# Kernel tuning notes

Measured on AMD Instinct MI355X. Metric: run time of the kernel, lower is better.

The kernel has to match this reference:

```python
import jax, jax.numpy as jnp
import numpy as np

_EPSILON = 1e-06

def _sparsemax(z):
    # sparsemax along last axis (Martins & Astudillo 2016, sort-based projection)
    m = z.shape[-1]
    z_sorted = jnp.flip(jnp.sort(z, axis=-1), axis=-1)          # descending
    z_cum = jnp.cumsum(z_sorted, axis=-1)
    r = jnp.arange(1, m + 1, dtype=z.dtype)
    support = (1.0 + r * z_sorted) > z_cum                       # [b, m]
    k = jnp.sum(support, axis=-1, keepdims=True)                 # support size, int
    tau = (jnp.take_along_axis(z_cum, k - 1, axis=-1) - 1.0) / k.astype(z.dtype)
    return jnp.maximum(z - tau, 0.0)

def setup_inputs() -> dict:
    key = jax.random.key(0)
    ks = jax.random.split(key, 4)
    b, m, d, out = 2048, 8192, 1024, 1000
    encoder_output = jax.random.normal(ks[0], (b, d), dtype=jnp.float32)
    memory_set = jax.random.normal(ks[1], (m, d), dtype=jnp.float32)
    W1 = jax.random.normal(ks[2], (d, 2 * d), dtype=jnp.float32) * (1.0 / np.sqrt(d))
    b1 = jnp.zeros((2 * d,), dtype=jnp.float32)
    W2 = jax.random.normal(ks[3], (2 * d, out), dtype=jnp.float32) * (1.0 / np.sqrt(2 * d))
    b2 = jnp.zeros((out,), dtype=jnp.float32)
    return {"encoder_output": encoder_output, "memory_set": memory_set,
            "W1": W1, "b1": b1, "W2": W2, "b2": b2}

def reference(encoder_output, memory_set, W1, b1, W2, b2):
    # cosine distance: 1 - x_hat @ y_hat^T  (with eps inside the sqrt, as in torch code)
    x_norm = encoder_output / jnp.sqrt(jnp.sum(encoder_output * encoder_output, axis=1, keepdims=True) + _EPSILON)
    y_norm = memory_set / jnp.sqrt(jnp.sum(memory_set * memory_set, axis=1, keepdims=True) + _EPSILON)
    dist = 1.0 - jnp.matmul(x_norm, y_norm.T)                    # [b, m]
    content_weights = _sparsemax(-dist)                          # [b, m]
    memory_vector = jnp.matmul(content_weights, memory_set)      # [b, d]
    h = jax.nn.relu(jnp.matmul(memory_vector, W1) + b1)          # [b, 2d]
    output = jnp.matmul(h, W2) + b2                              # [b, out]
    return output
```

## Files before the change

### kernel.cpp

```cpp
#include <hip/hip_runtime.h>
#include <hip/hip_bf16.h>


#define TPB 256
#define CAP 1024

typedef __bf16 bf16x8 __attribute__((ext_vector_type(8)));
typedef float  f32x4  __attribute__((ext_vector_type(4)));

typedef const __attribute__((address_space(1))) void* gas_ptr;
typedef __attribute__((address_space(3))) void*       las_ptr;

__device__ __forceinline__ unsigned short f2bf(float f) {
    __hip_bfloat16 h = __float2bfloat16(f);
    union { __hip_bfloat16 h; unsigned short s; } u; u.h = h; return u.s;
}

__device__ __forceinline__ float bf2f(unsigned short s) {
    union { unsigned int b; float f; } u; u.b = (unsigned int)s << 16; return u.f;
}

__device__ __forceinline__ float block_reduce_sum(float v, float* sred) {
    #pragma unroll
    for (int off = 32; off > 0; off >>= 1) v += __shfl_down(v, off, 64);
    int lane = threadIdx.x & 63;
    int wid  = threadIdx.x >> 6;
    if (lane == 0) sred[wid] = v;
    __syncthreads();
    if (threadIdx.x == 0) {
        float s = 0.f;
        for (int i = 0; i < 4; ++i) s += sred[i];
        sred[0] = s;
    }
    __syncthreads();
    float r = sred[0];
    __syncthreads();
    return r;
}

__device__ __forceinline__ void block_reduce_sum2(float& a, float& b, float* sred) {
    #pragma unroll
    for (int off = 32; off > 0; off >>= 1) {
        a += __shfl_down(a, off, 64);
        b += __shfl_down(b, off, 64);
    }
    int lane = threadIdx.x & 63, wid = threadIdx.x >> 6;
    if (lane == 0) { sred[wid] = a; sred[4 + wid] = b; }
    __syncthreads();
    if (threadIdx.x == 0) {
        sred[0] = sred[0] + sred[1] + sred[2] + sred[3];
        sred[4] = sred[4] + sred[5] + sred[6] + sred[7];
    }
    __syncthreads();
    a = sred[0]; b = sred[4];
    __syncthreads();
}

__global__ __launch_bounds__(TPB) void normalize_rows_bf16(const float* __restrict__ X,
                                                           unsigned short* __restrict__ Y,
                                                           float* __restrict__ norms,
                                                           int cols) {
    __shared__ float sred[4];
    int row = blockIdx.x, tid = threadIdx.x;
    const float4* x4 = (const float4*)(X + (size_t)row * cols);
    ushort4* y4 = (ushort4*)(Y + (size_t)row * cols);
    int n4 = cols >> 2;
    float ss = 0.f;
    for (int i = tid; i < n4; i += TPB) {
        float4 v = x4[i];
        ss += v.x * v.x + v.y * v.y + v.z * v.z + v.w * v.w;
    }
    float tot = block_reduce_sum(ss, sred);
    float nrm = sqrtf(tot + 1e-6f);
    float inv = 1.0f / nrm;
    if (norms && tid == 0) norms[row] = nrm;
    for (int i = tid; i < n4; i += TPB) {
        float4 v = x4[i];
        ushort4 o;
        o.x = f2bf(v.x * inv); o.y = f2bf(v.y * inv);
        o.z = f2bf(v.z * inv); o.w = f2bf(v.w * inv);
        y4[i] = o;
    }
}

__global__ __launch_bounds__(TPB) void transpose_cast(const float* __restrict__ in,
                                                      unsigned short* __restrict__ out,
                                                      int R, int C, int Cpad) {
    __shared__ float t[32][33];
    int x = threadIdx.x & 31, y = threadIdx.x >> 5;
    int r0 = blockIdx.y * 32, c0 = blockIdx.x * 32;
    #pragma unroll
    for (int yy = y; yy < 32; yy += 8) {
        int c = c0 + x;
        t[yy][x] = (c < C) ? in[(size_t)(r0 + yy) * C + c] : 0.f;
    }
    __syncthreads();
    #pragma unroll
    for (int yy = y; yy < 32; yy += 8) {
        int c = c0 + yy;
        if (c < Cpad)
            out[(size_t)c * R + r0 + x] = f2bf(t[x][yy]);
    }
}

__global__ __launch_bounds__(TPB) void sparsemax_compact(float* __restrict__ Z,
                                                         const float* __restrict__ ynorm,
                                                         int* __restrict__ cnt, int m) {
    __shared__ float sz[8192];
    __shared__ float sred[8];
    __shared__ unsigned short cidx[CAP];
    __shared__ float cval[CAP];
    __shared__ unsigned int lcnt, ocnt;
    int row = blockIdx.x, tid = threadIdx.x;
    float* zrow = Z + (size_t)row * m;
    unsigned int* prow = (unsigned int*)zrow;
    int n4 = m >> 2;
    float4* sz4 = (float4*)sz;
    const float4* zr4 = (const float4*)zrow;

    float s = 0.f, q = 0.f;
    for (int i = tid; i < n4; i += TPB) {
        float4 v = zr4[i];
        sz4[i] = v;
        s += v.x + v.y + v.z + v.w;
        q += v.x * v.x + v.y * v.y + v.z * v.z + v.w * v.w;
    }
    if (tid == 0) { lcnt = 0; ocnt = 0; }
    block_reduce_sum2(s, q, sred);
    float fm   = (float)m;
    float mean = s / fm;
    float sig  = sqrtf(fmaxf(q / fm - mean * mean, 0.f));
    float tau_s = (s - 1.f) / fm;
    float tau_g = mean + 2.f * sig;

    float Sg = 0.f, cg = 0.f, Ss = 0.f, cs = 0.f;
    for (int i = tid; i < m; i += TPB) {
        float z = sz[i];
        if (z > tau_g) { Sg += z - tau_g; cg += 1.f; }
        if (z > tau_s) { Ss += z - tau_s; cs += 1.f; }
    }
    block_reduce_sum2(Sg, cg, sred);
    block_reduce_sum2(Ss, cs, sred);

    float tau_lb, S_act, c_act;
    if (Sg >= 1.f) { tau_lb = tau_g; S_act = Sg + cg * tau_g; c_act = cg; }
    else           { tau_lb = tau_s; S_act = Ss + cs * tau_s; c_act = cs; }
    float tau1 = (S_act - 1.f) / c_act;
    if (tau1 < tau_lb) tau1 = tau_lb;

    for (int i = tid; i < m; i += TPB) {
        float z = sz[i];
        if (z > tau1) {
            unsigned int slot = atomicAdd(&lcnt, 1u);
            if (slot < CAP) { cidx[slot] = (unsigned short)i; cval[slot] = z; }
        }
    }
    __syncthreads();

    if (lcnt <= CAP && lcnt > 0) {
        int n = (int)lcnt;
        float tau = tau1, prev = -1.f;
        for (int it = 0; it < 64; ++it) {
            float S = 0.f, c = 0.f;
            for (int j = tid; j < n; j += TPB) {
                float z = cval[j];
                if (z > tau) { S += z; c += 1.f; }
            }
            block_reduce_sum2(S, c, sred);
            if (c < 0.5f || c == prev) break;
            tau = (S - 1.f) / c; prev = c;
        }
        for (int j = tid; j < n; j += TPB) {
            float w = cval[j] - tau;
            if (w > 0.f) {
                int idx = (int)cidx[j];
                unsigned int slot = atomicAdd(&ocnt, 1u);
                prow[slot] = ((unsigned int)idx << 16) | (unsigned int)f2bf(w * ynorm[idx]);
            }
        }
        __syncthreads();
        if (tid == 0) cnt[row] = (int)ocnt;
    } else {
        float tau = tau1, prev = -1.f;
        for (int it = 0; it < 64; ++it) {
            float S = 0.f, c = 0.f;
            for (int i = tid; i < m; i += TPB) {
                float z = sz[i];
                if (z > tau) { S += z; c += 1.f; }
            }
            block_reduce_sum2(S, c, sred);
            if (c < 0.5f || c == prev) break;
            tau = (S - 1.f) / c; prev = c;
        }
        for (int i = tid; i < m; i += TPB) {
            float w = sz[i] - tau;
            if (w > 0.f) {
                unsigned int slot = atomicAdd(&ocnt, 1u);
                prow[slot] = ((unsigned int)i << 16) | (unsigned int)f2bf(w * ynorm[i]);
            }
        }
        __syncthreads();
        if (tid == 0) cnt[row] = (int)ocnt;
    }
}

__global__ __launch_bounds__(TPB) void sparse_mv(const unsigned int* __restrict__ packed,
                                                 const int* __restrict__ cnt,
                                                 const unsigned short* __restrict__ yn,
                                                 unsigned short* __restrict__ mv,
                                                 int m, int d) {
    __shared__ unsigned int sl[TPB];
    int row = blockIdx.x, tid = threadIdx.x;
    const unsigned int* prow = packed + (size_t)row * m;
    int n = cnt[row];
    int c0 = tid * 4;
    float acc0 = 0.f, acc1 = 0.f, acc2 = 0.f, acc3 = 0.f;
    for (int j0 = 0; j0 < n; j0 += TPB) {
        int chunk = min(TPB, n - j0);
        __syncthreads();
        if (tid < chunk) sl[tid] = prow[j0 + tid];
        __syncthreads();
        #pragma unroll 4
        for (int jj = 0; jj < chunk; ++jj) {
            unsigned int u = sl[jj];
            int idx = (int)(u >> 16);
            float w = bf2f((unsigned short)(u & 0xffffu));
            ushort4 v = *(const ushort4*)&yn[(size_t)idx * d + c0];
            acc0 += w * bf2f(v.x);
            acc1 += w * bf2f(v.y);
            acc2 += w * bf2f(v.z);
            acc3 += w * bf2f(v.w);
        }
    }
    ushort4 o;
    o.x = f2bf(acc0); o.y = f2bf(acc1); o.z = f2bf(acc2); o.w = f2bf(acc3);
    *(ushort4*)&mv[(size_t)row * d + c0] = o;
}

template <int BN, int STORE_BF16, int RELU, int HASBIAS>
__global__ __launch_bounds__(TPB) void gemm_bt(const unsigned short* __restrict__ A,
                                               const unsigned short* __restrict__ B,
                                               const float* __restrict__ bias,
                                               void* __restrict__ C,
                                               int M, int K, int lda, int NOUT, int ldc) {
    constexpr int IT = (BN == 128) ? 4 : 2;
    __shared__ unsigned short lA[128 * 32];
    __shared__ unsigned short lB[BN * 32];
    int tid = threadIdx.x;
    int lane = tid & 63, wv = tid >> 6;
    int wm = (BN == 128) ? (wv & 1) * 64 : wv * 32;
    int wn = (BN == 128) ? (wv >> 1) * 64 : 0;
    int lr = lane & 15, kq = lane >> 4;

    int rowBase = blockIdx.y * 128;
    int colBase = blockIdx.x * BN;

    f32x4 acc[IT][4] = {};

    for (int k0 = 0; k0 < K; k0 += 32) {
        #pragma unroll
        for (int l = 0; l < 2; ++l) {
            int li = l * 256 + tid;
            int r = li >> 2, seg = li & 3;
            const char* g = (const char*)(A + (size_t)(rowBase + r) * lda + k0) + seg * 16;
            __builtin_amdgcn_global_load_lds((gas_ptr)g, (las_ptr)((char*)lA + li * 16), 16, 0, 0);
        }
        #pragma unroll
        for (int l = 0; l < BN / 64; ++l) {
            int li = l * 256 + tid;
            int r = li >> 2, seg = li & 3;
            const char* g = (const char*)(B + (size_t)(colBase + r) * K + k0) + seg * 16;
            __builtin_amdgcn_global_load_lds((gas_ptr)g, (las_ptr)((char*)lB + li * 16), 16, 0, 0);
        }
        __syncthreads();

        bf16x8 av[IT], bv[4];
        #pragma unroll
        for (int i = 0; i < IT; ++i)
            av[i] = *(const bf16x8*)&lA[(wm + i * 16 + lr) * 32 + kq * 8];
        #pragma unroll
        for (int j = 0; j < 4; ++j)
            bv[j] = *(const bf16x8*)&lB[(wn + j * 16 + lr) * 32 + kq * 8];
        #pragma unroll
        for (int i = 0; i < IT; ++i)
            #pragma unroll
            for (int j = 0; j < 4; ++j)
                acc[i][j] = __builtin_amdgcn_mfma_f32_16x16x32_bf16(av[i], bv[j], acc[i][j], 0, 0, 0);
        __syncthreads();
    }

    float* Cf = (float*)C;
    unsigned short* Cb = (unsigned short*)C;
    #pragma unroll
    for (int j = 0; j < 4; ++j) {
        int col = colBase + wn + j * 16 + lr;
        if (col >= NOUT) continue;
        float bv_ = HASBIAS ? bias[col] : 0.f;
        #pragma unroll
        for (int i = 0; i < IT; ++i) {
            #pragma unroll
            for (int r = 0; r < 4; ++r) {
                int row = rowBase + wm + i * 16 + kq * 4 + r;
                float v = acc[i][j][r] + bv_;
                if (RELU) v = fmaxf(v, 0.f);
                if (STORE_BF16) Cb[(size_t)row * ldc + col] = f2bf(v);
                else            Cf[(size_t)row * ldc + col] = v;
            }
        }
    }
}

extern "C" void kernel_launch(void* const* d_in, const int* in_sizes, int n_in,
                              void* d_out, int out_size, void* d_ws, size_t ws_size,
                              hipStream_t stream) {
    const float* enc = (const float*)d_in[0];
    const float* mem = (const float*)d_in[1];
    const float* W1  = (const float*)d_in[2];
    const float* b1  = (const float*)d_in[3];
    const float* W2  = (const float*)d_in[4];
    const float* b2  = (const float*)d_in[5];

    const int d    = in_sizes[3] / 2;
    const int b    = in_sizes[0] / d;
    const int m    = in_sizes[1] / d;
    const int d2   = in_sizes[3];
    const int outN = in_sizes[5];
    const int outPad = 1024;

    unsigned short* xn    = (unsigned short*)d_ws;
    unsigned short* yn    = xn  + (size_t)b * d;
    float*          ynorm = (float*)(yn + (size_t)m * d);
    unsigned short* W1T   = (unsigned short*)(ynorm + m);
    unsigned short* W2T   = W1T + (size_t)d2 * d;
    float*          Z     = (float*)(W2T + (size_t)outPad * d2);
    int*            cnt   = (int*)(Z + (size_t)b * m);
    unsigned short* mv    = (unsigned short*)(cnt + b);
    unsigned short* h     = mv + (size_t)b * d;

    normalize_rows_bf16<<<b, TPB, 0, stream>>>(enc, xn, nullptr, d);
    normalize_rows_bf16<<<m, TPB, 0, stream>>>(mem, yn, ynorm, d);

    transpose_cast<<<dim3(d2 / 32, d / 32), TPB, 0, stream>>>(W1, W1T, d, d2, d2);
    transpose_cast<<<dim3(outPad / 32, d2 / 32), TPB, 0, stream>>>(W2, W2T, d2, outN, outPad);

    gemm_bt<128, 0, 0, 0><<<dim3(m / 128, b / 128), TPB, 0, stream>>>(xn, yn, nullptr, Z,
                                                                      b, d, d, m, m);
    sparsemax_compact<<<b, TPB, 0, stream>>>(Z, ynorm, cnt, m);

    sparse_mv<<<b, TPB, 0, stream>>>((const unsigned int*)Z, cnt, yn, mv, m, d);

    gemm_bt<64, 1, 1, 1><<<dim3(d2 / 64, b / 128), TPB, 0, stream>>>(mv, W1T, b1, h,
                                                                     b, d, d, d2, d2);
    gemm_bt<64, 0, 0, 1><<<dim3(outPad / 64, b / 128), TPB, 0, stream>>>(h, W2T, b2, d_out,
                                                                         b, d2, d2, outN, outN);
}
```

Baseline: 302.3 us.

## Store similarity matrix in fp16, widen GEMM K-tile with swizzled LDS, merge normalize launches

The similarity GEMM now writes its output as fp16 instead of fp32, halving the write and re-read traffic of the large b×m intermediate. The sparsemax kernel reads it as packed halves, and the sparse-mv pitch is adjusted because the packed index/weight list now lives in the fp16 buffer. The GEMM K-tile grows from 32 to 64, with an XOR swizzle on the LDS layout to avoid bank conflicts, and the two row-normalize launches are merged into one. fp16 rounding of the similarity scores may shift sparsemax support decisions. The packed output rows are also half as long, so a row with a large support could overflow its buffer.

```diff
diff --git a/kernel.cpp b/kernel.cpp
--- a/kernel.cpp
+++ b/kernel.cpp
@@ -4,6 +4,7 @@
 
 #define TPB 256
 #define CAP 1024
+#define BK 64
 
 typedef __bf16 bf16x8 __attribute__((ext_vector_type(8)));
 typedef float  f32x4  __attribute__((ext_vector_type(4)));
@@ -15,23 +16,23 @@
     __hip_bfloat16 h = __float2bfloat16(f);
     union { __hip_bfloat16 h; unsigned short s; } u; u.h = h; return u.s;
 }
-
 __device__ __forceinline__ float bf2f(unsigned short s) {
     union { unsigned int b; float f; } u; u.b = (unsigned int)s << 16; return u.f;
 }
+__device__ __forceinline__ unsigned short f2h(float f) {
+    union { _Float16 h; unsigned short s; } u; u.h = (_Float16)f; return u.s;
+}
+__device__ __forceinline__ float h2f(unsigned short s) {
+    union { unsigned short s; _Float16 h; } u; u.s = s; return (float)u.h;
+}
 
 __device__ __forceinline__ float block_reduce_sum(float v, float* sred) {
     #pragma unroll
     for (int off = 32; off > 0; off >>= 1) v += __shfl_down(v, off, 64);
-    int lane = threadIdx.x & 63;
-    int wid  = threadIdx.x >> 6;
+    int lane = threadIdx.x & 63, wid = threadIdx.x >> 6;
     if (lane == 0) sred[wid] = v;
     __syncthreads();
-    if (threadIdx.x == 0) {
-        float s = 0.f;
-        for (int i = 0; i < 4; ++i) s += sred[i];
-        sred[0] = s;
-    }
+    if (threadIdx.x == 0) sred[0] = sred[0] + sred[1] + sred[2] + sred[3];
     __syncthreads();
     float r = sred[0];
     __syncthreads();
@@ -56,12 +57,17 @@
     __syncthreads();
 }
 
-__global__ __launch_bounds__(TPB) void normalize_rows_bf16(const float* __restrict__ X,
-                                                           unsigned short* __restrict__ Y,
-                                                           float* __restrict__ norms,
-                                                           int cols) {
+__global__ __launch_bounds__(TPB) void normalize_rows_bf16(const float* __restrict__ X0,
+                                                           unsigned short* __restrict__ Y0,
+                                                           const float* __restrict__ X1,
+                                                           unsigned short* __restrict__ Y1,
+                                                           float* __restrict__ norms1,
+                                                           int nrow0, int cols) {
     __shared__ float sred[4];
-    int row = blockIdx.x, tid = threadIdx.x;
+    int r = blockIdx.x, tid = threadIdx.x;
+    const float* X; unsigned short* Y; float* nn; int row;
+    if (r < nrow0) { X = X0; Y = Y0; nn = nullptr; row = r; }
+    else           { X = X1; Y = Y1; nn = norms1; row = r - nrow0; }
     const float4* x4 = (const float4*)(X + (size_t)row * cols);
     ushort4* y4 = (ushort4*)(Y + (size_t)row * cols);
     int n4 = cols >> 2;
@@ -73,7 +79,7 @@
     float tot = block_reduce_sum(ss, sred);
     float nrm = sqrtf(tot + 1e-6f);
     float inv = 1.0f / nrm;
-    if (norms && tid == 0) norms[row] = nrm;
+    if (nn && tid == 0) nn[row] = nrm;
     for (int i = tid; i < n4; i += TPB) {
         float4 v = x4[i];
         ushort4 o;
@@ -103,7 +109,7 @@
     }
 }
 
-__global__ __launch_bounds__(TPB) void sparsemax_compact(float* __restrict__ Z,
+__global__ __launch_bounds__(TPB) void sparsemax_compact(unsigned short* __restrict__ Zh,
                                                          const float* __restrict__ ynorm,
                                                          int* __restrict__ cnt, int m) {
     __shared__ float sz[8192];
@@ -112,18 +118,24 @@
     __shared__ float cval[CAP];
     __shared__ unsigned int lcnt, ocnt;
     int row = blockIdx.x, tid = threadIdx.x;
-    float* zrow = Z + (size_t)row * m;
+    unsigned short* zrow = Zh + (size_t)row * m;
     unsigned int* prow = (unsigned int*)zrow;
-    int n4 = m >> 2;
+    const uint4* zr8 = (const uint4*)zrow;
+    int n8 = m >> 3;
+
+    float s = 0.f, q = 0.f;
     float4* sz4 = (float4*)sz;
-    const float4* zr4 = (const float4*)zrow;
-
-    float s = 0.f, q = 0.f;
-    for (int i = tid; i < n4; i += TPB) {
-        float4 v = zr4[i];
-        sz4[i] = v;
-        s += v.x + v.y + v.z + v.w;
-        q += v.x * v.x + v.y * v.y + v.z * v.z + v.w * v.w;
+    for (int i = tid; i < n8; i += TPB) {
+        uint4 v = zr8[i];
+        float4 a, bq;
+        a.x = h2f((unsigned short)(v.x & 0xffffu)); a.y = h2f((unsigned short)(v.x >> 16));
+        a.z = h2f((unsigned short)(v.y & 0xffffu)); a.w = h2f((unsigned short)(v.y >> 16));
+        bq.x = h2f((unsigned short)(v.z & 0xffffu)); bq.y = h2f((unsigned short)(v.z >> 16));
+        bq.z = h2f((unsigned short)(v.w & 0xffffu)); bq.w = h2f((unsigned short)(v.w >> 16));
+        sz4[2 * i] = a; sz4[2 * i + 1] = bq;
+        s += a.x + a.y + a.z + a.w + bq.x + bq.y + bq.z + bq.w;
+        q += a.x * a.x + a.y * a.y + a.z * a.z + a.w * a.w
+           + bq.x * bq.x + bq.y * bq.y + bq.z * bq.z + bq.w * bq.w;
     }
     if (tid == 0) { lcnt = 0; ocnt = 0; }
     block_reduce_sum2(s, q, sred);
@@ -208,10 +220,10 @@
                                                  const int* __restrict__ cnt,
                                                  const unsigned short* __restrict__ yn,
                                                  unsigned short* __restrict__ mv,
-                                                 int m, int d) {
+                                                 int pitchU, int d) {
     __shared__ unsigned int sl[TPB];
     int row = blockIdx.x, tid = threadIdx.x;
-    const unsigned int* prow = packed + (size_t)row * m;
+    const unsigned int* prow = packed + (size_t)row * pitchU;
     int n = cnt[row];
     int c0 = tid * 4;
     float acc0 = 0.f, acc1 = 0.f, acc2 = 0.f, acc3 = 0.f;
@@ -237,15 +249,15 @@
     *(ushort4*)&mv[(size_t)row * d + c0] = o;
 }
 
-template <int BN, int STORE_BF16, int RELU, int HASBIAS>
+template <int BN, int OUTMODE, int RELU, int HASBIAS>
 __global__ __launch_bounds__(TPB) void gemm_bt(const unsigned short* __restrict__ A,
                                                const unsigned short* __restrict__ B,
                                                const float* __restrict__ bias,
                                                void* __restrict__ C,
                                                int M, int K, int lda, int NOUT, int ldc) {
     constexpr int IT = (BN == 128) ? 4 : 2;
-    __shared__ unsigned short lA[128 * 32];
-    __shared__ unsigned short lB[BN * 32];
+    __shared__ unsigned short lA[128 * BK];
+    __shared__ unsigned short lB[BN * BK];
     int tid = threadIdx.x;
     int lane = tid & 63, wv = tid >> 6;
     int wm = (BN == 128) ? (wv & 1) * 64 : wv * 32;
@@ -257,35 +269,46 @@
 
     f32x4 acc[IT][4] = {};
 
-    for (int k0 = 0; k0 < K; k0 += 32) {
+    for (int k0 = 0; k0 < K; k0 += BK) {
         #pragma unroll
-        for (int l = 0; l < 2; ++l) {
+        for (int l = 0; l < 4; ++l) {
             int li = l * 256 + tid;
-            int r = li >> 2, seg = li & 3;
-            const char* g = (const char*)(A + (size_t)(rowBase + r) * lda + k0) + seg * 16;
+            int row = li >> 3, s0 = li & 7;
+            int seg = s0 ^ (row & 7);
+            const char* g = (const char*)(A + (size_t)(rowBase + row) * lda + k0) + seg * 16;
             __builtin_amdgcn_global_load_lds((gas_ptr)g, (las_ptr)((char*)lA + li * 16), 16, 0, 0);
         }
         #pragma unroll
-        for (int l = 0; l < BN / 64; ++l) {
+        for (int l = 0; l < BN / 32; ++l) {
             int li = l * 256 + tid;
-            int r = li >> 2, seg = li & 3;
-            const char* g = (const char*)(B + (size_t)(colBase + r) * K + k0) + seg * 16;
+            int row = li >> 3, s0 = li & 7;
+            int seg = s0 ^ (row & 7);
+            const char* g = (const char*)(B + (size_t)(colBase + row) * K + k0) + seg * 16;
             __builtin_amdgcn_global_load_lds((gas_ptr)g, (las_ptr)((char*)lB + li * 16), 16, 0, 0);
         }
         __syncthreads();
 
-        bf16x8 av[IT], bv[4];
         #pragma unroll
-        for (int i = 0; i < IT; ++i)
-            av[i] = *(const bf16x8*)&lA[(wm + i * 16 + lr) * 32 + kq * 8];
-        #pragma unroll
-        for (int j = 0; j < 4; ++j)
-            bv[j] = *(const bf16x8*)&lB[(wn + j * 16 + lr) * 32 + kq * 8];
-        #pragma unroll
-        for (int i = 0; i < IT; ++i)
+        for (int h = 0; h < 2; ++h) {
+            bf16x8 av[IT], bv[4];
             #pragma unroll
-            for (int j = 0; j < 4; ++j)
-                acc[i][j] = __builtin_amdgcn_mfma_f32_16x16x32_bf16(av[i], bv[j], acc[i][j], 0, 0, 0);
+            for (int i = 0; i < IT; ++i) {
+                int row = wm + i * 16 + lr;
+                av[i] = *(const bf16x8*)((const char*)lA + row * 128
+                                         + ((((h << 2) | kq) ^ (row & 7)) * 16));
+            }
+            #pragma unroll
+            for (int j = 0; j < 4; ++j) {
+                int row = wn + j * 16 + lr;
+                bv[j] = *(const bf16x8*)((const char*)lB + row * 128
+                                         + ((((h << 2) | kq) ^ (row & 7)) * 16));
+            }
+            #pragma unroll
+            for (int i = 0; i < IT; ++i)
+                #pragma unroll
+                for (int j = 0; j < 4; ++j)
+                    acc[i][j] = __builtin_amdgcn_mfma_f32_16x16x32_bf16(av[i], bv[j], acc[i][j], 0, 0, 0);
+        }
         __syncthreads();
     }
 
@@ -303,8 +326,9 @@
                 int row = rowBase + wm + i * 16 + kq * 4 + r;
                 float v = acc[i][j][r] + bv_;
                 if (RELU) v = fmaxf(v, 0.f);
-                if (STORE_BF16) Cb[(size_t)row * ldc + col] = f2bf(v);
-                else            Cf[(size_t)row * ldc + col] = v;
+                if (OUTMODE == 0)      Cf[(size_t)row * ldc + col] = v;
+                else if (OUTMODE == 1) Cb[(size_t)row * ldc + col] = f2bf(v);
+                else                   Cb[(size_t)row * ldc + col] = f2h(v);
             }
         }
     }
@@ -332,22 +356,21 @@
     float*          ynorm = (float*)(yn + (size_t)m * d);
     unsigned short* W1T   = (unsigned short*)(ynorm + m);
     unsigned short* W2T   = W1T + (size_t)d2 * d;
-    float*          Z     = (float*)(W2T + (size_t)outPad * d2);
-    int*            cnt   = (int*)(Z + (size_t)b * m);
+    unsigned short* Zh    = W2T + (size_t)outPad * d2;
+    int*            cnt   = (int*)(Zh + (size_t)b * m);
     unsigned short* mv    = (unsigned short*)(cnt + b);
     unsigned short* h     = mv + (size_t)b * d;
 
-    normalize_rows_bf16<<<b, TPB, 0, stream>>>(enc, xn, nullptr, d);
-    normalize_rows_bf16<<<m, TPB, 0, stream>>>(mem, yn, ynorm, d);
+    normalize_rows_bf16<<<b + m, TPB, 0, stream>>>(enc, xn, mem, yn, ynorm, b, d);
 
     transpose_cast<<<dim3(d2 / 32, d / 32), TPB, 0, stream>>>(W1, W1T, d, d2, d2);
     transpose_cast<<<dim3(outPad / 32, d2 / 32), TPB, 0, stream>>>(W2, W2T, d2, outN, outPad);
 
-    gemm_bt<128, 0, 0, 0><<<dim3(m / 128, b / 128), TPB, 0, stream>>>(xn, yn, nullptr, Z,
+    gemm_bt<128, 2, 0, 0><<<dim3(m / 128, b / 128), TPB, 0, stream>>>(xn, yn, nullptr, Zh,
                                                                       b, d, d, m, m);
-    sparsemax_compact<<<b, TPB, 0, stream>>>(Z, ynorm, cnt, m);
-
-    sparse_mv<<<b, TPB, 0, stream>>>((const unsigned int*)Z, cnt, yn, mv, m, d);
+    sparsemax_compact<<<b, TPB, 0, stream>>>(Zh, ynorm, cnt, m);
+
+    sparse_mv<<<b, TPB, 0, stream>>>((const unsigned int*)Zh, cnt, yn, mv, m / 2, d);
 
     gemm_bt<64, 1, 1, 1><<<dim3(d2 / 64, b / 128), TPB, 0, stream>>>(mv, W1T, b1, h,
                                                                      b, d, d, d2, d2);
```

After: 275.9 us. -8.7%, faster.
